# Kernel optimization log

Hardware: AMD Instinct MI355X
Metric: run time of the kernel (lower is better)

Reference implementation:

```python
import jax, jax.numpy as jnp
import numpy as np

B, S, H = 4, 2048, 1024
E = 8
INTER = 2816  # round(4.0*1024*2/3)=2731 -> next multiple of 256


def setup_inputs() -> dict:
    key = jax.random.key(0)
    k1, k2, k3, k4 = jax.random.split(key, 4)
    x = jax.random.normal(k1, (B, S, H), dtype=jnp.float32)
    gate_w = jax.random.normal(k2, (E, H), dtype=jnp.float32) * 0.02
    w_gate_up = jax.random.normal(k3, (E, H, 2 * INTER), dtype=jnp.float32) * 0.02
    w_down = jax.random.normal(k4, (E, INTER, H), dtype=jnp.float32) * 0.02
    return {"x": x, "gate_w": gate_w, "w_gate_up": w_gate_up, "w_down": w_down, "top_k": 2}


def _moe(x, gate_w, w_gate_up, w_down, top_k):
    Bx, Sx, Hx = x.shape
    Ex = gate_w.shape[0]
    T = Bx * Sx
    # Router
    logits = jnp.einsum('bsh,eh->bse', x, gate_w)
    probs = jax.nn.softmax(logits.astype(jnp.float32), axis=-1)  # [B,S,E] fp32
    topk_vals, topk_idx = jax.lax.top_k(probs, top_k)             # [B,S,K]
    topk_w = topk_vals / jnp.clip(topk_vals.sum(-1, keepdims=True), 1e-8)
    importance = probs.mean((0, 1))                               # [E]
    onehot = jax.nn.one_hot(topk_idx, Ex, dtype=probs.dtype)      # [B,S,K,E]
    sel_mask = onehot.sum(-2)                                     # [B,S,E] 0/1 (topk unique)
    load = sel_mask.sum((0, 1)) / (T * top_k)
    aux_loss = (Ex * (importance * load)).sum()
    # Dense combine weights per token/expert (scatter_add equivalent)
    W_full = (onehot * topk_w[..., None]).sum(-2)                 # [B,S,E]
    x_flat = x.reshape(T, Hx)
    W_flat = W_full.reshape(T, Ex).astype(x.dtype)
    out = jnp.zeros_like(x_flat)
    for e in range(Ex):  # fixed small expert loop
        gu = x_flat @ w_gate_up[e]                                # [T, 2I]
        g, u = jnp.split(gu, 2, axis=-1)
        y = (jax.nn.silu(g) * u) @ w_down[e]                      # [T, H]
        out = out + y * W_flat[:, e:e + 1]
    return out.reshape(Bx, Sx, Hx), aux_loss


def reference(x, gate_w, w_gate_up, w_down, top_k):
    return _moe(x, gate_w, w_gate_up, w_down, int(top_k))
```

## Files before the change

### kernel.cpp

```cpp
#include <hip/hip_runtime.h>

#define E_ 8
#define H_ 1024
#define I_ 2816
#define GU_ 5632
#define T_ 8192
#define NBR_ 2048

typedef __attribute__((ext_vector_type(8))) __bf16 bf16x8;
typedef __attribute__((ext_vector_type(4))) float f32x4;
typedef __attribute__((ext_vector_type(8))) unsigned short u16x8;
typedef __attribute__((ext_vector_type(4))) unsigned short u16x4;
typedef unsigned short u16;

__device__ __forceinline__ float bf2f(u16 u) {
  union { unsigned int i; float f; } v; v.i = ((unsigned int)u) << 16; return v.f;
}
__device__ __forceinline__ u16 f2bf(float f) {
  union { float f; unsigned int i; } v; v.f = f;
  unsigned int r = v.i + 0x7fffu + ((v.i >> 16) & 1u);
  return (u16)(r >> 16);
}
__device__ __forceinline__ void gld16(const void* g, void* l) {
  __builtin_amdgcn_global_load_lds((const __attribute__((address_space(1))) void*)g,
                                   (__attribute__((address_space(3))) void*)l, 16, 0, 0);
}

#define BAR() __builtin_amdgcn_s_barrier()
#define VMC(n) asm volatile("s_waitcnt vmcnt(" #n ")" ::: "memory")

__global__ __launch_bounds__(256) void k_router(
    const float* __restrict__ x, const float* __restrict__ gw,
    float* __restrict__ part_imp, int* __restrict__ part_cnt,
    int* __restrict__ tok_e, float* __restrict__ tok_w,
    u16* __restrict__ xb)
{
  __shared__ float s_imp[8];
  __shared__ int s_cnt[8];
  if (threadIdx.x < 8) { s_imp[threadIdx.x] = 0.f; s_cnt[threadIdx.x] = 0; }
  __syncthreads();

  const int t = blockIdx.x * 4 + (threadIdx.x >> 6);
  const int lane = threadIdx.x & 63;
  const float* xr = x + (size_t)t * H_;
  const f32x4* xp = (const f32x4*)(xr + lane * 16);
  f32x4 v0 = xp[0], v1 = xp[1], v2 = xp[2], v3 = xp[3];
  float xv[16];
#pragma unroll
  for (int b = 0; b < 4; ++b) { xv[b] = v0[b]; xv[4+b] = v1[b]; xv[8+b] = v2[b]; xv[12+b] = v3[b]; }
  u16x8 o0, o1;
#pragma unroll
  for (int j = 0; j < 8; ++j) { o0[j] = f2bf(xv[j]); o1[j] = f2bf(xv[8 + j]); }
  *(u16x8*)(xb + (size_t)t * H_ + lane * 16) = o0;
  *(u16x8*)(xb + (size_t)t * H_ + lane * 16 + 8) = o1;

  float lg[8];
#pragma unroll
  for (int e = 0; e < 8; ++e) {
    const f32x4* gp = (const f32x4*)(gw + e * H_ + lane * 16);
    float s = 0.f;
#pragma unroll
    for (int a = 0; a < 4; ++a) {
      f32x4 g4 = gp[a];
#pragma unroll
      for (int b = 0; b < 4; ++b) s += xv[a * 4 + b] * g4[b];
    }
    lg[e] = s;
  }
#pragma unroll
  for (int e = 0; e < 8; ++e)
#pragma unroll
    for (int off = 32; off; off >>= 1) lg[e] += __shfl_xor(lg[e], off);

  float m = lg[0];
#pragma unroll
  for (int e = 1; e < 8; ++e) m = fmaxf(m, lg[e]);
  float p[8], sum = 0.f;
#pragma unroll
  for (int e = 0; e < 8; ++e) { p[e] = __expf(lg[e] - m); sum += p[e]; }
  float inv = 1.f / sum;
#pragma unroll
  for (int e = 0; e < 8; ++e) p[e] *= inv;
  int e0 = 0;
#pragma unroll
  for (int e = 1; e < 8; ++e) if (p[e] > p[e0]) e0 = e;
  int e1 = (e0 == 0) ? 1 : 0;
#pragma unroll
  for (int e = 0; e < 8; ++e) if (e != e0 && p[e] > p[e1]) e1 = e;
  float d = 1.f / (p[e0] + p[e1]);
  if (lane == 0) {
#pragma unroll
    for (int e = 0; e < 8; ++e) atomicAdd(&s_imp[e], p[e]);
    atomicAdd(&s_cnt[e0], 1);
    atomicAdd(&s_cnt[e1], 1);
    tok_e[2 * t] = e0; tok_e[2 * t + 1] = e1;
    tok_w[2 * t] = p[e0] * d; tok_w[2 * t + 1] = p[e1] * d;
  }
  __syncthreads();
  if (threadIdx.x < 8) {
    part_imp[blockIdx.x * 8 + threadIdx.x] = s_imp[threadIdx.x];
    part_cnt[blockIdx.x * 8 + threadIdx.x] = s_cnt[threadIdx.x];
  }
}

__global__ __launch_bounds__(512) void k_reduce_scan(
    const float* __restrict__ part_imp, const int* __restrict__ part_cnt,
    int* __restrict__ counts, int* __restrict__ offsets, float* __restrict__ out)
{
  const int w = threadIdx.x >> 6, lane = threadIdx.x & 63;
  float si = 0.f; int sc = 0;
  for (int b = lane; b < NBR_; b += 64) { si += part_imp[b * 8 + w]; sc += part_cnt[b * 8 + w]; }
#pragma unroll
  for (int off = 32; off; off >>= 1) { si += __shfl_xor(si, off); sc += __shfl_xor(sc, off); }
  __shared__ float fimp[8];
  __shared__ int fcnt[8];
  if (lane == 0) { fimp[w] = si; fcnt[w] = sc; }
  __syncthreads();
  if (threadIdx.x == 0) {
    int off = 0; float aux = 0.f;
#pragma unroll
    for (int e = 0; e < 8; ++e) {
      counts[e] = fcnt[e]; offsets[e] = off; off += fcnt[e];
      aux += fimp[e] * (float)fcnt[e];
    }
    out[(size_t)T_ * H_] = 8.f * aux / ((float)T_ * (float)(2 * T_));
  }
}

__global__ __launch_bounds__(256) void k_scatter(
    const int* __restrict__ tok_e, const float* __restrict__ tok_w,
    const int* __restrict__ offsets, int* __restrict__ cursors,
    int* __restrict__ rows, float* __restrict__ wslot, int* __restrict__ t2s)
{
  __shared__ int lcnt[8], lbase[8];
  if (threadIdx.x < 8) lcnt[threadIdx.x] = 0;
  __syncthreads();
  const int t = blockIdx.x * 256 + threadIdx.x;
  const int e0 = tok_e[2 * t], e1 = tok_e[2 * t + 1];
  const int p0 = atomicAdd(&lcnt[e0], 1);
  const int p1 = atomicAdd(&lcnt[e1], 1);
  __syncthreads();
  if (threadIdx.x < 8) lbase[threadIdx.x] = atomicAdd(&cursors[threadIdx.x], lcnt[threadIdx.x]);
  __syncthreads();
  const int s0 = offsets[e0] + lbase[e0] + p0;
  const int s1 = offsets[e1] + lbase[e1] + p1;
  rows[s0] = t; wslot[s0] = tok_w[2 * t];     t2s[2 * t] = s0;
  rows[s1] = t; wslot[s1] = tok_w[2 * t + 1]; t2s[2 * t + 1] = s1;
}

__global__ __launch_bounds__(256) void k_transpose(
    const float* __restrict__ src, u16* __restrict__ dst, int R, int C)
{
  __shared__ float tile[64][68];
  const int z = blockIdx.z;
  const int c0 = blockIdx.x * 64, r0 = blockIdx.y * 64;
  const float* s = src + (size_t)z * R * C;
  u16* d = dst + (size_t)z * R * C;
  const int tx = threadIdx.x & 15, ty = threadIdx.x >> 4;
#pragma unroll
  for (int i = 0; i < 4; ++i) {
    f32x4 v = *(const f32x4*)(s + (size_t)(r0 + ty + i * 16) * C + c0 + tx * 4);
    *(f32x4*)(&tile[ty + i * 16][tx * 4]) = v;
  }
  __syncthreads();
  const int c = threadIdx.x >> 2, rq = threadIdx.x & 3;
#pragma unroll
  for (int j = 0; j < 4; ++j) {
    u16x4 w;
#pragma unroll
    for (int m = 0; m < 4; ++m) w[m] = f2bf(tile[rq * 16 + j * 4 + m][c]);
    *(u16x4*)(&d[(size_t)(c0 + c) * R + r0 + rq * 16 + j * 4]) = w;
  }
}

__global__ __launch_bounds__(512, 2) void k_gemm1(
    const u16* __restrict__ xb, const u16* __restrict__ wgu_t,
    const int* __restrict__ counts, const int* __restrict__ offsets,
    const int* __restrict__ rows, const float* __restrict__ wslot,
    u16* __restrict__ act)
{
  extern __shared__ char sh[];
  const int bid = blockIdx.x;
  const int l = (bid & 7) * 704 + (bid >> 3);
  const int e = l / 704;
  const int rm = l - e * 704;
  const int yb = rm >> 5, xx = rm & 31;
  const int cnt = counts[e];
  const int m0 = xx * 256;
  if (m0 >= cnt) return;
  const int seg = offsets[e];
  const int segLast = seg + cnt - 1;
  const int n0 = yb * 128;

  const int tid = threadIdx.x;
  const int wid = tid >> 6, lane = tid & 63;
  const int srow = tid >> 3;
  const int scol = (((tid & 7) ^ (srow & 7)) * 8);

  const u16* wge = wgu_t + (size_t)e * GU_ * H_;

  const u16* aPtr[4];
#pragma unroll
  for (int i = 0; i < 4; ++i) {
    int slot = seg + m0 + i * 64 + srow;
    aPtr[i] = xb + (size_t)rows[slot > segLast ? segLast : slot] * H_ + scol;
  }
  const u16* bPtr[4];
#pragma unroll
  for (int i = 0; i < 4; ++i) {
    int r = i * 64 + srow;
    int gr = (r < 128) ? (n0 + r) : (I_ + n0 + (r - 128));
    bPtr[i] = wge + (size_t)gr * H_ + scol;
  }

  const int wm = (wid >> 2) * 128;
  const int wn = (wid & 3) * 32;

  f32x4 accg[8][2], accu[8][2];
#pragma unroll
  for (int i = 0; i < 8; ++i)
#pragma unroll
    for (int j = 0; j < 2; ++j) { accg[i][j] = (f32x4){0.f,0.f,0.f,0.f}; accu[i][j] = (f32x4){0.f,0.f,0.f,0.f}; }

#define STAGE_A1(b, kt) { const int k0 = (kt) * 64;                               \
    char* dst = sh + (b) * 65536 + tid * 16;                                      \
    _Pragma("unroll") for (int i = 0; i < 4; ++i) gld16(aPtr[i] + k0, dst + i * 8192); }
#define STAGE_B1(b, kt) { const int k0 = (kt) * 64;                               \
    char* dst = sh + (b) * 65536 + 32768 + tid * 16;                              \
    _Pragma("unroll") for (int i = 0; i < 4; ++i) gld16(bPtr[i] + k0, dst + i * 8192); }

  const int NT = H_ / 64;
  STAGE_A1(0, 0); STAGE_B1(0, 0); STAGE_A1(1, 1);
  VMC(4);
  BAR();

  int cur = 0;
#pragma unroll 2
  for (int t = 0; t < NT; ++t) {
    STAGE_B1(cur ^ 1, (t + 1 < NT) ? t + 1 : NT - 1);
    const u16* As = (const u16*)(sh + cur * 65536);
    const u16* Bs = As + 16384;
#pragma unroll
    for (int ks = 0; ks < 2; ++ks) {
      const int koff = (ks * 32 + (lane >> 4) * 8) ^ ((lane & 7) * 8);
      bf16x8 a[8], bg[2], bu[2];
#pragma unroll
      for (int mf = 0; mf < 8; ++mf)
        a[mf] = *(const bf16x8*)(As + (wm + mf * 16 + (lane & 15)) * 64 + koff);
#pragma unroll
      for (int nf = 0; nf < 2; ++nf) {
        bg[nf] = *(const bf16x8*)(Bs + (wn + nf * 16 + (lane & 15)) * 64 + koff);
        bu[nf] = *(const bf16x8*)(Bs + (128 + wn + nf * 16 + (lane & 15)) * 64 + koff);
      }
      __builtin_amdgcn_s_setprio(1);
#pragma unroll
      for (int mf = 0; mf < 8; ++mf)
#pragma unroll
        for (int nf = 0; nf < 2; ++nf) {
          accg[mf][nf] = __builtin_amdgcn_mfma_f32_16x16x32_bf16(a[mf], bg[nf], accg[mf][nf], 0, 0, 0);
          accu[mf][nf] = __builtin_amdgcn_mfma_f32_16x16x32_bf16(a[mf], bu[nf], accu[mf][nf], 0, 0, 0);
        }
      __builtin_amdgcn_s_setprio(0);
    }
    asm volatile("" ::: "memory");
    BAR();
    STAGE_A1(cur, (t + 2 < NT) ? t + 2 : NT - 1);
    VMC(4);
    BAR();
    cur ^= 1;
  }
  VMC(0);
#undef STAGE_A1
#undef STAGE_B1

#pragma unroll
  for (int mf = 0; mf < 8; ++mf)
#pragma unroll
    for (int reg = 0; reg < 4; ++reg) {
      const int r = wm + mf * 16 + (lane >> 4) * 4 + reg;
      if (m0 + r >= cnt) continue;
      const int slot = seg + m0 + r;
      const float w = wslot[slot];
#pragma unroll
      for (int nf = 0; nf < 2; ++nf) {
        float g = accg[mf][nf][reg];
        float u = accu[mf][nf][reg];
        float sv = (g / (1.f + __expf(-g))) * u * w;
        act[(size_t)slot * I_ + n0 + wn + nf * 16 + (lane & 15)] = f2bf(sv);
      }
    }
}

__global__ __launch_bounds__(512, 2) void k_gemm2(
    const u16* __restrict__ act, const u16* __restrict__ wd_t,
    const int* __restrict__ counts, const int* __restrict__ offsets,
    u16* __restrict__ y)
{
  extern __shared__ char sh[];
  const int bid = blockIdx.x;
  const int l = (bid & 7) * 128 + (bid >> 3);
  const int e = l >> 7;
  const int rm = l & 127;
  const int yb = rm >> 5, xx = rm & 31;
  const int cnt = counts[e];
  const int m0 = xx * 256;
  if (m0 >= cnt) return;
  const int seg = offsets[e];
  const int segLast = seg + cnt - 1;
  const int n0 = yb * 256;

  const int tid = threadIdx.x;
  const int wid = tid >> 6, lane = tid & 63;
  const int srow = tid >> 3;
  const int scol = (((tid & 7) ^ (srow & 7)) * 8);

  const u16* wde = wd_t + (size_t)e * H_ * I_;

  const u16* aPtr[4];
#pragma unroll
  for (int i = 0; i < 4; ++i) {
    int slot = seg + m0 + i * 64 + srow;
    aPtr[i] = act + (size_t)(slot > segLast ? segLast : slot) * I_ + scol;
  }
  const u16* bPtr[4];
#pragma unroll
  for (int i = 0; i < 4; ++i)
    bPtr[i] = wde + (size_t)(n0 + i * 64 + srow) * I_ + scol;

  const int wm = (wid >> 2) * 128;
  const int wn = (wid & 3) * 64;

  f32x4 acc[8][4];
#pragma unroll
  for (int i = 0; i < 8; ++i)
#pragma unroll
    for (int j = 0; j < 4; ++j) acc[i][j] = (f32x4){0.f,0.f,0.f,0.f};

#define STAGE_A2(b, kt) { const int k0 = (kt) * 64;                               \
    char* dst = sh + (b) * 65536 + tid * 16;                                      \
    _Pragma("unroll") for (int i = 0; i < 4; ++i) gld16(aPtr[i] + k0, dst + i * 8192); }
#define STAGE_B2(b, kt) { const int k0 = (kt) * 64;                               \
    char* dst = sh + (b) * 65536 + 32768 + tid * 16;                              \
    _Pragma("unroll") for (int i = 0; i < 4; ++i) gld16(bPtr[i] + k0, dst + i * 8192); }

  const int NT = I_ / 64;
  STAGE_A2(0, 0); STAGE_B2(0, 0); STAGE_A2(1, 1);
  VMC(4);
  BAR();

  int cur = 0;
#pragma unroll 2
  for (int t = 0; t < NT; ++t) {
    STAGE_B2(cur ^ 1, (t + 1 < NT) ? t + 1 : NT - 1);
    const u16* As = (const u16*)(sh + cur * 65536);
    const u16* Bs = As + 16384;
#pragma unroll
    for (int ks = 0; ks < 2; ++ks) {
      const int koff = (ks * 32 + (lane >> 4) * 8) ^ ((lane & 7) * 8);
      bf16x8 a[8], b[4];
#pragma unroll
      for (int mf = 0; mf < 8; ++mf)
        a[mf] = *(const bf16x8*)(As + (wm + mf * 16 + (lane & 15)) * 64 + koff);
#pragma unroll
      for (int nf = 0; nf < 4; ++nf)
        b[nf] = *(const bf16x8*)(Bs + (wn + nf * 16 + (lane & 15)) * 64 + koff);
      __builtin_amdgcn_s_setprio(1);
#pragma unroll
      for (int mf = 0; mf < 8; ++mf)
#pragma unroll
        for (int nf = 0; nf < 4; ++nf)
          acc[mf][nf] = __builtin_amdgcn_mfma_f32_16x16x32_bf16(a[mf], b[nf], acc[mf][nf], 0, 0, 0);
      __builtin_amdgcn_s_setprio(0);
    }
    asm volatile("" ::: "memory");
    BAR();
    STAGE_A2(cur, (t + 2 < NT) ? t + 2 : NT - 1);
    VMC(4);
    BAR();
    cur ^= 1;
  }
  VMC(0);
#undef STAGE_A2
#undef STAGE_B2

#pragma unroll
  for (int mf = 0; mf < 8; ++mf)
#pragma unroll
    for (int reg = 0; reg < 4; ++reg) {
      const int r = wm + mf * 16 + (lane >> 4) * 4 + reg;
      if (m0 + r >= cnt) continue;
      const int slot = seg + m0 + r;
#pragma unroll
      for (int nf = 0; nf < 4; ++nf)
        y[(size_t)slot * H_ + n0 + wn + nf * 16 + (lane & 15)] = f2bf(acc[mf][nf][reg]);
    }
}

__global__ __launch_bounds__(256) void k_combine(
    const u16* __restrict__ y, const int* __restrict__ t2s, float* __restrict__ out)
{
  const size_t idx = ((size_t)blockIdx.x * 256 + threadIdx.x) * 8;
  const int t = (int)(idx >> 10);
  const int h = (int)(idx & 1023);
  const int s0 = t2s[2 * t], s1 = t2s[2 * t + 1];
  u16x8 a = *(const u16x8*)(y + (size_t)s0 * H_ + h);
  u16x8 b = *(const u16x8*)(y + (size_t)s1 * H_ + h);
  f32x4 o0, o1;
#pragma unroll
  for (int j = 0; j < 4; ++j) o0[j] = bf2f(a[j]) + bf2f(b[j]);
#pragma unroll
  for (int j = 0; j < 4; ++j) o1[j] = bf2f(a[4 + j]) + bf2f(b[4 + j]);
  *(f32x4*)(out + idx) = o0;
  *(f32x4*)(out + idx + 4) = o1;
}

extern "C" void kernel_launch(void* const* d_in, const int* in_sizes, int n_in,
                              void* d_out, int out_size, void* d_ws, size_t ws_size,
                              hipStream_t stream)
{
  const float* x   = (const float*)d_in[0];
  const float* gw  = (const float*)d_in[1];
  const float* wgu = (const float*)d_in[2];
  const float* wd  = (const float*)d_in[3];
  float* out = (float*)d_out;
  char* ws = (char*)d_ws;

  const size_t off_wgu_t = 0;
  const size_t off_wd_t  = off_wgu_t + (size_t)E_ * GU_ * H_ * 2;
  const size_t off_xb    = off_wd_t  + (size_t)E_ * H_ * I_ * 2;
  const size_t off_act   = off_xb    + (size_t)T_ * H_ * 2;
  const size_t off_ctrl  = off_act   + (size_t)2 * T_ * I_ * 2;
  const size_t need = off_ctrl + 128 + 5 * 65536;
  if (ws_size < need) return;

  u16* wgu_t = (u16*)(ws + off_wgu_t);
  u16* wd_t  = (u16*)(ws + off_wd_t);
  u16* xb    = (u16*)(ws + off_xb);
  u16* act   = (u16*)(ws + off_act);
  u16* y     = (u16*)(ws + off_wgu_t);
  float* part_imp = (float*)(ws + off_act);
  int*   part_cnt = (int*)(ws + off_act + (size_t)NBR_ * 8 * 4);
  char* ctrl = ws + off_ctrl;
  int*   counts  = (int*)(ctrl + 0);
  int*   cursors = (int*)(ctrl + 32);
  int*   offsets = (int*)(ctrl + 64);
  int*   tok_e   = (int*)(ctrl + 128);
  float* tok_w   = (float*)(ctrl + 128 + 1 * 65536);
  int*   rows    = (int*)(ctrl + 128 + 2 * 65536);
  float* wslot   = (float*)(ctrl + 128 + 3 * 65536);
  int*   t2s     = (int*)(ctrl + 128 + 4 * 65536);

  static bool attr_done = false;
  if (!attr_done) {
    hipFuncSetAttribute((const void*)k_gemm1, hipFuncAttributeMaxDynamicSharedMemorySize, 131072);
    hipFuncSetAttribute((const void*)k_gemm2, hipFuncAttributeMaxDynamicSharedMemorySize, 131072);
    attr_done = true;
  }

  hipMemsetAsync(ctrl, 0, 96, stream);
  hipLaunchKernelGGL(k_transpose, dim3(GU_ / 64, H_ / 64, E_), dim3(256), 0, stream, wgu, wgu_t, H_, GU_);
  hipLaunchKernelGGL(k_transpose, dim3(H_ / 64, I_ / 64, E_), dim3(256), 0, stream, wd, wd_t, I_, H_);
  hipLaunchKernelGGL(k_router, dim3(NBR_), dim3(256), 0, stream, x, gw, part_imp, part_cnt, tok_e, tok_w, xb);
  hipLaunchKernelGGL(k_reduce_scan, dim3(1), dim3(512), 0, stream, part_imp, part_cnt, counts, offsets, out);
  hipLaunchKernelGGL(k_scatter, dim3(T_ / 256), dim3(256), 0, stream, tok_e, tok_w, offsets, cursors, rows, wslot, t2s);
  hipLaunchKernelGGL(k_gemm1, dim3(32 * (I_ / 128) * E_), dim3(512), 131072, stream, xb, wgu_t, counts, offsets, rows, wslot, act);
  hipLaunchKernelGGL(k_gemm2, dim3(32 * (H_ / 256) * E_), dim3(512), 131072, stream, act, wd_t, counts, offsets, y);
  hipLaunchKernelGGL(k_combine, dim3((T_ * H_) / (256 * 8)), dim3(256), 0, stream, y, t2s, out);
}
```

Baseline: 542.6 us.

## Fuse expert combine into down-projection epilogue using fp32 atomic adds

Removes the separate combine kernel and the bf16 per-slot y buffer. Each gemm2 output row now looks up its token index and atomically adds its fp32 accumulator into the final output, which is zeroed by a memset at the start. This avoids writing and re-reading the intermediate y tensor and drops one launch, along with the t2s index bookkeeping in the scatter kernel. The cost is the output memset plus scattered fp32 global atomics in the GEMM epilogue. With exactly two adds onto zero per element, the result stays order-independent.

Result: slower. 589.1 us (+8.6%).

```diff
diff --git a/kernel.cpp b/kernel.cpp
--- a/kernel.cpp
+++ b/kernel.cpp
@@ -130,7 +130,7 @@
 __global__ __launch_bounds__(256) void k_scatter(
     const int* __restrict__ tok_e, const float* __restrict__ tok_w,
     const int* __restrict__ offsets, int* __restrict__ cursors,
-    int* __restrict__ rows, float* __restrict__ wslot, int* __restrict__ t2s)
+    int* __restrict__ rows, float* __restrict__ wslot)
 {
   __shared__ int lcnt[8], lbase[8];
   if (threadIdx.x < 8) lcnt[threadIdx.x] = 0;
@@ -144,8 +144,8 @@
   __syncthreads();
   const int s0 = offsets[e0] + lbase[e0] + p0;
   const int s1 = offsets[e1] + lbase[e1] + p1;
-  rows[s0] = t; wslot[s0] = tok_w[2 * t];     t2s[2 * t] = s0;
-  rows[s1] = t; wslot[s1] = tok_w[2 * t + 1]; t2s[2 * t + 1] = s1;
+  rows[s0] = t; wslot[s0] = tok_w[2 * t];
+  rows[s1] = t; wslot[s1] = tok_w[2 * t + 1];
 }
 
 __global__ __launch_bounds__(256) void k_transpose(
@@ -294,7 +294,7 @@
 __global__ __launch_bounds__(512, 2) void k_gemm2(
     const u16* __restrict__ act, const u16* __restrict__ wd_t,
     const int* __restrict__ counts, const int* __restrict__ offsets,
-    u16* __restrict__ y)
+    const int* __restrict__ rows, float* __restrict__ out)
 {
   extern __shared__ char sh[];
   const int bid = blockIdx.x;
@@ -390,28 +390,12 @@
       const int r = wm + mf * 16 + (lane >> 4) * 4 + reg;
       if (m0 + r >= cnt) continue;
       const int slot = seg + m0 + r;
+      const int token = rows[slot];
+      float* orow = out + (size_t)token * H_ + n0 + wn + (lane & 15);
 #pragma unroll
       for (int nf = 0; nf < 4; ++nf)
-        y[(size_t)slot * H_ + n0 + wn + nf * 16 + (lane & 15)] = f2bf(acc[mf][nf][reg]);
-    }
-}
-
-__global__ __launch_bounds__(256) void k_combine(
-    const u16* __restrict__ y, const int* __restrict__ t2s, float* __restrict__ out)
-{
-  const size_t idx = ((size_t)blockIdx.x * 256 + threadIdx.x) * 8;
-  const int t = (int)(idx >> 10);
-  const int h = (int)(idx & 1023);
-  const int s0 = t2s[2 * t], s1 = t2s[2 * t + 1];
-  u16x8 a = *(const u16x8*)(y + (size_t)s0 * H_ + h);
-  u16x8 b = *(const u16x8*)(y + (size_t)s1 * H_ + h);
-  f32x4 o0, o1;
-#pragma unroll
-  for (int j = 0; j < 4; ++j) o0[j] = bf2f(a[j]) + bf2f(b[j]);
-#pragma unroll
-  for (int j = 0; j < 4; ++j) o1[j] = bf2f(a[4 + j]) + bf2f(b[4 + j]);
-  *(f32x4*)(out + idx) = o0;
-  *(f32x4*)(out + idx + 4) = o1;
+        atomicAdd(orow + nf * 16, acc[mf][nf][reg]);
+    }
 }
 
 extern "C" void kernel_launch(void* const* d_in, const int* in_sizes, int n_in,
@@ -430,14 +414,13 @@
   const size_t off_xb    = off_wd_t  + (size_t)E_ * H_ * I_ * 2;
   const size_t off_act   = off_xb    + (size_t)T_ * H_ * 2;
   const size_t off_ctrl  = off_act   + (size_t)2 * T_ * I_ * 2;
-  const size_t need = off_ctrl + 128 + 5 * 65536;
+  const size_t need = off_ctrl + 128 + 4 * 65536;
   if (ws_size < need) return;
 
   u16* wgu_t = (u16*)(ws + off_wgu_t);
   u16* wd_t  = (u16*)(ws + off_wd_t);
   u16* xb    = (u16*)(ws + off_xb);
   u16* act   = (u16*)(ws + off_act);
-  u16* y     = (u16*)(ws + off_wgu_t);
   float* part_imp = (float*)(ws + off_act);
   int*   part_cnt = (int*)(ws + off_act + (size_t)NBR_ * 8 * 4);
   char* ctrl = ws + off_ctrl;
@@ -448,7 +431,6 @@
   float* tok_w   = (float*)(ctrl + 128 + 1 * 65536);
   int*   rows    = (int*)(ctrl + 128 + 2 * 65536);
   float* wslot   = (float*)(ctrl + 128 + 3 * 65536);
-  int*   t2s     = (int*)(ctrl + 128 + 4 * 65536);
 
   static bool attr_done = false;
   if (!attr_done) {
@@ -457,13 +439,13 @@
     attr_done = true;
   }
 
+  hipMemsetAsync(out, 0, (size_t)out_size * sizeof(float), stream);
   hipMemsetAsync(ctrl, 0, 96, stream);
   hipLaunchKernelGGL(k_transpose, dim3(GU_ / 64, H_ / 64, E_), dim3(256), 0, stream, wgu, wgu_t, H_, GU_);
   hipLaunchKernelGGL(k_transpose, dim3(H_ / 64, I_ / 64, E_), dim3(256), 0, stream, wd, wd_t, I_, H_);
   hipLaunchKernelGGL(k_router, dim3(NBR_), dim3(256), 0, stream, x, gw, part_imp, part_cnt, tok_e, tok_w, xb);
   hipLaunchKernelGGL(k_reduce_scan, dim3(1), dim3(512), 0, stream, part_imp, part_cnt, counts, offsets, out);
-  hipLaunchKernelGGL(k_scatter, dim3(T_ / 256), dim3(256), 0, stream, tok_e, tok_w, offsets, cursors, rows, wslot, t2s);
+  hipLaunchKernelGGL(k_scatter, dim3(T_ / 256), dim3(256), 0, stream, tok_e, tok_w, offsets, cursors, rows, wslot);
   hipLaunchKernelGGL(k_gemm1, dim3(32 * (I_ / 128) * E_), dim3(512), 131072, stream, xb, wgu_t, counts, offsets, rows, wslot, act);
-  hipLaunchKernelGGL(k_gemm2, dim3(32 * (H_ / 256) * E_), dim3(512), 131072, stream, act, wd_t, counts, offsets, y);
-  hipLaunchKernelGGL(k_combine, dim3((T_ * H_) / (256 * 8)), dim3(256), 0, stream, y, t2s, out);
-}
+  hipLaunchKernelGGL(k_gemm2, dim3(32 * (H_ / 256) * E_), dim3(512), 131072, stream, act, wd_t, counts, offsets, rows, out);
+}
```
